# Performance work log

Hardware: AMD Instinct MI355X
Metric: run time of the kernel (lower is better)

Reference implementation:

```python
import jax, jax.numpy as jnp
import numpy as np

B, T, I, H, TGT = 256, 4096, 8, 32, 8


def setup_inputs() -> dict:
    key = jax.random.key(0)
    ks = jax.random.split(key, 6)
    return {
        "inputs": jax.random.normal(ks[0], (B, T, I), jnp.float32),
        "encode_weights": jax.random.normal(ks[1], (H, I), jnp.float32) * 0.3,   # xavier-ish
        "w_ih": jax.random.normal(ks[2], (3 * H, H), jnp.float32) * 0.1,        # GRU weight_ih_l0
        "w_hh": jax.random.normal(ks[3], (3 * H, H), jnp.float32) * 0.1,        # GRU weight_hh_l0
        "b_ih": jax.random.normal(ks[4], (3 * H,), jnp.float32) * 0.1,
        "b_hh": jax.random.normal(ks[5], (3 * H,), jnp.float32) * 0.1,
    }


def _gru(gx_t, w_hh, b_hh, h0):
    # gx_t: time-major input-gate pre-activations [T, B, 3H]; PyTorch GRU math:
    # r = sig(gx_r + gh_r); z = sig(gx_z + gh_z); n = tanh(gx_n + r*gh_n); h = (1-z)*n + z*h
    Hd = h0.shape[-1]
    def step(h, gx):
        gh = h @ w_hh.T + b_hh                      # [B, 3H]
        r = jax.nn.sigmoid(gx[..., :Hd] + gh[..., :Hd])
        z = jax.nn.sigmoid(gx[..., Hd:2 * Hd] + gh[..., Hd:2 * Hd])
        n = jnp.tanh(gx[..., 2 * Hd:] + r * gh[..., 2 * Hd:])
        h_new = (1.0 - z) * n + z * h
        return h_new, h_new
    _, hs = jax.lax.scan(step, h0, gx_t)            # hs: [T, B, H]
    return hs


def reference(inputs, encode_weights, w_ih, w_hh, b_ih, b_hh):
    # encode = F.linear(inputs, encode_weights)
    encode = jnp.einsum('bti,hi->bth', inputs, encode_weights)      # [B, T, H]
    gx = jnp.einsum('bth,gh->btg', encode, w_ih) + b_ih             # [B, T, 3H]
    gx_t = jnp.swapaxes(gx, 0, 1)                                   # [T, B, 3H]
    h0 = jnp.zeros((inputs.shape[0], encode_weights.shape[0]), inputs.dtype)
    latents = jnp.swapaxes(_gru(gx_t, w_hh, b_hh, h0), 0, 1)        # [B, T, H]
    # tied decoder: F.linear(latents, encode_weights[:, :target_size].T)
    outputs = jnp.einsum('bth,ho->bto', latents, encode_weights[:, :TGT])
    return outputs, latents
```

## Files before the change

kernel.cpp:

```cpp
#include <hip/hip_runtime.h>
#include <hip/hip_bf16.h>
#include <cstdint>
#include <cstddef>

#define Bsz  256
#define Tn   4096
#define In   8
#define Hn   32
#define TGTn 8

typedef float v2f __attribute__((ext_vector_type(2)));

__device__ __forceinline__ v2f pk_fma(v2f a, v2f b, v2f c) {
    return __builtin_elementwise_fma(a, b, c);
}
__device__ __forceinline__ v2f pk_mul(v2f a, v2f b) { return a * b; }

template<int N>
__device__ __forceinline__ float dpp_ror(float x) {
    int xi = __float_as_int(x);
    int r = __builtin_amdgcn_update_dpp(xi, xi, 0x120 + N, 0xF, 0xF, false);
    return __int_as_float(r);
}

__device__ __forceinline__ float half_sum(float x) {
    auto r = __builtin_amdgcn_permlane32_swap(__float_as_int(x), __float_as_int(x),
                                              false, false);
    return __int_as_float((int)r[0]) + __int_as_float((int)r[1]);
}

__device__ __forceinline__ void row16_pair(float x, float& a_out, float& b_out) {
    auto r = __builtin_amdgcn_permlane16_swap(__float_as_int(x), __float_as_int(x),
                                              false, false);
    a_out = __int_as_float((int)r[0]);
    b_out = __int_as_float((int)r[1]);
}

__device__ __forceinline__ void gather16_probe(float v, v2f H[8]) {
    v2f G0; G0.x = v;                G0.y = dpp_ror<1>(v);
    v2f G1; G1.x = dpp_ror<2>(G0.x); G1.y = dpp_ror<2>(G0.y);
    v2f G2; G2.x = dpp_ror<4>(G0.x); G2.y = dpp_ror<4>(G0.y);
    v2f G3; G3.x = dpp_ror<4>(G1.x); G3.y = dpp_ror<4>(G1.y);
    v2f G4; G4.x = dpp_ror<8>(G0.x); G4.y = dpp_ror<8>(G0.y);
    v2f G5; G5.x = dpp_ror<8>(G1.x); G5.y = dpp_ror<8>(G1.y);
    v2f G6; G6.x = dpp_ror<8>(G2.x); G6.y = dpp_ror<8>(G2.y);
    v2f G7; G7.x = dpp_ror<8>(G3.x); G7.y = dpp_ror<8>(G3.y);
    H[0]=G0; H[1]=G1; H[2]=G2; H[3]=G3; H[4]=G4; H[5]=G5; H[6]=G6; H[7]=G7;
}

__device__ __forceinline__ float rcpf(float x) { return __builtin_amdgcn_rcpf(x); }
__device__ __forceinline__ float sigm(float x) { return rcpf(1.f + __expf(-x)); }
__device__ __forceinline__ float tanhfast(float x) {
    float e = __expf(2.f * x);
    return 1.f - 2.f * rcpf(e + 1.f);
}

__global__ void fuse_wih_kernel(const float* __restrict__ w_ih,
                                const float* __restrict__ E,
                                float* __restrict__ Wf) {
    int tid = threadIdx.x;
    int g = tid >> 3, i = tid & 7;
    float acc = 0.f;
#pragma unroll
    for (int k = 0; k < Hn; ++k)
        acc = fmaf(w_ih[g * Hn + k], E[k * In + i], acc);
    Wf[g * In + i] = acc;
}

#define GRU_STEP(XNEXT, XREFILL, DO_REFILL)                                          \
  {                                                                                  \
    v2f ar0 = pk_fma(H0, whr0, pk_fma(H2, whr2, pk_fma(H4, whr4, pk_mul(H6, whr6))));\
    v2f ar1 = pk_fma(H1, whr1, pk_fma(H3, whr3, pk_fma(H5, whr5, pk_mul(H7, whr7))));\
    v2f az0 = pk_fma(H0, whz0, pk_fma(H2, whz2, pk_fma(H4, whz4, pk_mul(H6, whz6))));\
    v2f az1 = pk_fma(H1, whz1, pk_fma(H3, whz3, pk_fma(H5, whz5, pk_mul(H7, whz7))));\
    v2f an0 = pk_fma(H0, whn0, pk_fma(H2, whn2, pk_fma(H4, whn4, pk_mul(H6, whn6))));\
    v2f an1 = pk_fma(H1, whn1, pk_fma(H3, whn3, pk_fma(H5, whn5, pk_mul(H7, whn7))));\
    v2f art = ar0 + ar1;                                                             \
    v2f azt = az0 + az1;                                                             \
    v2f ant = an0 + an1;                                                             \
    float pr  = art.x + art.y + axr;                                                 \
    float pz  = azt.x + azt.y + axz;                                                 \
    float phn = ant.x + ant.y + bhnh;                                                \
    float cr  = half_sum(pr);                                                        \
    float cz  = half_sum(pz);                                                        \
    float chn = half_sum(phn);                                                       \
    float r = sigm(cr);                                                              \
    float z = sigm(cz);                                                              \
    float n = tanhfast(cxn + r * chn);                                               \
    hj = __builtin_fmaf(z, hj - n, n);                                               \
    float va, vb;                                                                    \
    row16_pair(hj, va, vb);                                                          \
    float gv = pick_a ? va : vb;                        \
    H0 = v2f{gv, dpp_ror<1>(gv)};                                                    \
    H1 = v2f{dpp_ror<2>(H0.x), dpp_ror<2>(H0.y)};                                    \
    H2 = v2f{dpp_ror<4>(H0.x), dpp_ror<4>(H0.y)};                                    \
    H3 = v2f{dpp_ror<4>(H1.x), dpp_ror<4>(H1.y)};                                    \
    H4 = v2f{dpp_ror<8>(H0.x), dpp_ror<8>(H0.y)};                                    \
    H5 = v2f{dpp_ror<8>(H1.x), dpp_ror<8>(H1.y)};                                    \
    H6 = v2f{dpp_ror<8>(H2.x), dpp_ror<8>(H2.y)};                                    \
    H7 = v2f{dpp_ror<8>(H3.x), dpp_ror<8>(H3.y)};                                    \
    *latp = hj;                                                                      \
    latp += Hn;                                                                      \
    {                                                                                \
      v2f nx0 = v2f{XNEXT.x, XNEXT.y}, nx1 = v2f{XNEXT.z, XNEXT.w};                  \
      v2f ta = pk_fma(nx0, wxr0, pk_mul(nx1, wxr1));                                 \
      axr = ta.x + ta.y + brh;                                                       \
      v2f tb = pk_fma(nx0, wxz0, pk_mul(nx1, wxz1));                                 \
      axz = tb.x + tb.y + bzh;                                                       \
      v2f tc = pk_fma(nx0, wxn0, pk_mul(nx1, wxn1));                                 \
      cxn = half_sum(tc.x + tc.y + bxnh);                                            \
    }                                                                                \
    if (DO_REFILL) { XREFILL = *(const float4*)refp; refp += In; }                   \
  }

#define KEEP(v) asm volatile("" : "+v"(v))
__attribute__((amdgpu_flat_work_group_size(64, 64), amdgpu_waves_per_eu(1, 1)))
__global__ void gru_kernel(const float* __restrict__ x,
                           const float* __restrict__ Wf,
                           const float* __restrict__ w_hh,
                           const float* __restrict__ b_ih,
                           const float* __restrict__ b_hh,
                           float* __restrict__ latents) {
    const int lane = threadIdx.x & 63;
    const int grp  = lane >> 5;
    const int j    = lane & 31;
    const int r16  = lane & 15;
    const int b    = blockIdx.x;

    int sidx[16];
    {
        v2f P[8];
        gather16_probe((float)r16, P);
#pragma unroll
        for (int q = 0; q < 8; ++q) {
            sidx[2*q]   = (int)P[q].x;
            sidx[2*q+1] = (int)P[q].y;
        }
    }
    bool pick_a;
    {
        float va, vb;
        row16_pair((float)j, va, vb);
        pick_a = ((int)va == grp * 16 + r16);
    }

    v2f whr0, whr1, whr2, whr3, whr4, whr5, whr6, whr7;
    v2f whz0, whz1, whz2, whz3, whz4, whz5, whz6, whz7;
    v2f whn0, whn1, whn2, whn3, whn4, whn5, whn6, whn7;
#define LOADW(Q)                                                                  \
    {                                                                             \
        const int c0 = grp * 16 + sidx[2*Q], c1 = grp * 16 + sidx[2*Q+1];         \
        whr##Q = v2f{w_hh[(0*Hn + j)*Hn + c0], w_hh[(0*Hn + j)*Hn + c1]};         \
        whz##Q = v2f{w_hh[(1*Hn + j)*Hn + c0], w_hh[(1*Hn + j)*Hn + c1]};         \
        whn##Q = v2f{w_hh[(2*Hn + j)*Hn + c0], w_hh[(2*Hn + j)*Hn + c1]};         \
        KEEP(whr##Q); KEEP(whz##Q); KEEP(whn##Q);                                 \
    }
    LOADW(0) LOADW(1) LOADW(2) LOADW(3) LOADW(4) LOADW(5) LOADW(6) LOADW(7)
#undef LOADW

    v2f wxr0 = v2f{Wf[(0*Hn+j)*In + grp*4 + 0], Wf[(0*Hn+j)*In + grp*4 + 1]};
    v2f wxr1 = v2f{Wf[(0*Hn+j)*In + grp*4 + 2], Wf[(0*Hn+j)*In + grp*4 + 3]};
    v2f wxz0 = v2f{Wf[(1*Hn+j)*In + grp*4 + 0], Wf[(1*Hn+j)*In + grp*4 + 1]};
    v2f wxz1 = v2f{Wf[(1*Hn+j)*In + grp*4 + 2], Wf[(1*Hn+j)*In + grp*4 + 3]};
    v2f wxn0 = v2f{Wf[(2*Hn+j)*In + grp*4 + 0], Wf[(2*Hn+j)*In + grp*4 + 1]};
    v2f wxn1 = v2f{Wf[(2*Hn+j)*In + grp*4 + 2], Wf[(2*Hn+j)*In + grp*4 + 3]};
    KEEP(wxr0); KEEP(wxr1); KEEP(wxz0); KEEP(wxz1); KEEP(wxn0); KEEP(wxn1);

    float brh  = 0.5f * (b_ih[j]        + b_hh[j]);
    float bzh  = 0.5f * (b_ih[Hn + j]   + b_hh[Hn + j]);
    float bxnh = 0.5f * b_ih[2*Hn + j];
    float bhnh = 0.5f * b_hh[2*Hn + j];
    KEEP(brh); KEEP(bzh); KEEP(bxnh); KEEP(bhnh);

    const float* xb = x + (size_t)b * Tn * In;
    float* latp     = latents + (size_t)b * Tn * Hn + j;
    const float* refp = xb + (size_t)8 * In + grp * 4;

    float hj = 0.f;
    v2f H0{0.f,0.f}, H1{0.f,0.f}, H2{0.f,0.f}, H3{0.f,0.f},
        H4{0.f,0.f}, H5{0.f,0.f}, H6{0.f,0.f}, H7{0.f,0.f};

    float4 x0 = *(const float4*)&xb[0*In + grp*4];
    float4 x1 = *(const float4*)&xb[1*In + grp*4];
    float4 x2 = *(const float4*)&xb[2*In + grp*4];
    float4 x3 = *(const float4*)&xb[3*In + grp*4];
    float4 x4 = *(const float4*)&xb[4*In + grp*4];
    float4 x5 = *(const float4*)&xb[5*In + grp*4];
    float4 x6 = *(const float4*)&xb[6*In + grp*4];
    float4 x7 = *(const float4*)&xb[7*In + grp*4];

    float axr, axz, cxn;
    {
        v2f nx0 = v2f{x0.x, x0.y}, nx1 = v2f{x0.z, x0.w};
        v2f ta = pk_fma(nx0, wxr0, pk_mul(nx1, wxr1));
        axr = ta.x + ta.y + brh;
        v2f tb = pk_fma(nx0, wxz0, pk_mul(nx1, wxz1));
        axz = tb.x + tb.y + bzh;
        v2f tc = pk_fma(nx0, wxn0, pk_mul(nx1, wxn1));
        cxn = half_sum(tc.x + tc.y + bxnh);
    }

#pragma unroll 1
    for (int s0 = 0; s0 < Tn - 8; s0 += 8) {
        GRU_STEP(x1, x0, true)
        GRU_STEP(x2, x1, true)
        GRU_STEP(x3, x2, true)
        GRU_STEP(x4, x3, true)
        GRU_STEP(x5, x4, true)
        GRU_STEP(x6, x5, true)
        GRU_STEP(x7, x6, true)
        GRU_STEP(x0, x7, true)
    }
    GRU_STEP(x1, x0, false)
    GRU_STEP(x2, x1, false)
    GRU_STEP(x3, x2, false)
    GRU_STEP(x4, x3, false)
    GRU_STEP(x5, x4, false)
    GRU_STEP(x6, x5, false)
    GRU_STEP(x7, x6, false)
    GRU_STEP(x0, x7, false)
}
#undef KEEP

__global__ void decode_kernel(const float* __restrict__ lat,
                              const float* __restrict__ E,
                              float* __restrict__ out) {
    __shared__ float ldsE[Hn * TGTn];
    int tid = threadIdx.x;
    if (tid < Hn * TGTn) ldsE[tid] = E[tid];
    __syncthreads();
    size_t idx = (size_t)blockIdx.x * 256 + tid;
    int o      = (int)(idx & (TGTn - 1));
    size_t row = idx >> 3;
    const float* lrow = lat + row * Hn;
    float acc = 0.f;
#pragma unroll
    for (int h = 0; h < Hn; ++h)
        acc = fmaf(lrow[h], ldsE[h * TGTn + o], acc);
    out[idx] = acc;
}

extern "C" void kernel_launch(void* const* d_in, const int* in_sizes, int n_in,
                              void* d_out, int out_size, void* d_ws, size_t ws_size,
                              hipStream_t stream) {
    const float* x    = (const float*)d_in[0];
    const float* E    = (const float*)d_in[1];
    const float* w_ih = (const float*)d_in[2];
    const float* w_hh = (const float*)d_in[3];
    const float* b_ih = (const float*)d_in[4];
    const float* b_hh = (const float*)d_in[5];

    float* out = (float*)d_out;
    float* lat = out + (size_t)Bsz * Tn * TGTn;
    float* Wf  = (float*)d_ws;

    fuse_wih_kernel<<<1, 768, 0, stream>>>(w_ih, E, Wf);
    gru_kernel<<<Bsz, 64, 0, stream>>>(x, Wf, w_hh, b_ih, b_hh, lat);
    decode_kernel<<<(Bsz * Tn * TGTn) / 256, 256, 0, stream>>>(lat, E, out);
}
```

Baseline: 992.5 us.

## Prescale GRU weights for exp2 activations and compute full input preact per lane

Folds the -log2(e) and 2*log2(e) factors into w_hh, the fused input weights and the biases, so sigmoid and tanh become a raw exp2 plus reciprocal with no extra multiply. Each lane now computes the full 8-wide input pre-activation itself rather than splitting it across the two half-waves and combining with a permlane swap. That removes one cross-lane swap from the serial recurrence, at the cost of more FMAs and twice the x loads per lane. The x prefetch ring shrinks from 8 to 4 timesteps, which lowers register use but shortens the load lead time.

```diff
diff --git a/kernel.cpp b/kernel.cpp
--- a/kernel.cpp
+++ b/kernel.cpp
@@ -9,12 +9,21 @@
 #define Hn   32
 #define TGTn 8
 
+#define ALPHA (-1.44269504088896341f)
+#define BETA  ( 2.88539008177792682f)
+
 typedef float v2f __attribute__((ext_vector_type(2)));
 
 __device__ __forceinline__ v2f pk_fma(v2f a, v2f b, v2f c) {
     return __builtin_elementwise_fma(a, b, c);
 }
-__device__ __forceinline__ v2f pk_mul(v2f a, v2f b) { return a * b; }
+
+#if __has_builtin(__builtin_amdgcn_exp2f)
+__device__ __forceinline__ float exp2f_fast(float x) { return __builtin_amdgcn_exp2f(x); }
+#else
+__device__ __forceinline__ float exp2f_fast(float x) { return __expf(x * 0.69314718056f); }
+#endif
+__device__ __forceinline__ float rcpf(float x) { return __builtin_amdgcn_rcpf(x); }
 
 template<int N>
 __device__ __forceinline__ float dpp_ror(float x) {
@@ -48,13 +57,6 @@
     H[0]=G0; H[1]=G1; H[2]=G2; H[3]=G3; H[4]=G4; H[5]=G5; H[6]=G6; H[7]=G7;
 }
 
-__device__ __forceinline__ float rcpf(float x) { return __builtin_amdgcn_rcpf(x); }
-__device__ __forceinline__ float sigm(float x) { return rcpf(1.f + __expf(-x)); }
-__device__ __forceinline__ float tanhfast(float x) {
-    float e = __expf(2.f * x);
-    return 1.f - 2.f * rcpf(e + 1.f);
-}
-
 __global__ void fuse_wih_kernel(const float* __restrict__ w_ih,
                                 const float* __restrict__ E,
                                 float* __restrict__ Wf) {
@@ -64,29 +66,40 @@
 #pragma unroll
     for (int k = 0; k < Hn; ++k)
         acc = fmaf(w_ih[g * Hn + k], E[k * In + i], acc);
-    Wf[g * In + i] = acc;
-}
-
-#define GRU_STEP(XNEXT, XREFILL, DO_REFILL)                                          \
+    Wf[g * In + i] = acc * (g < 2 * Hn ? ALPHA : BETA);
+}
+
+#define PREACT(XA, XB)                                                               \
   {                                                                                  \
-    v2f ar0 = pk_fma(H0, whr0, pk_fma(H2, whr2, pk_fma(H4, whr4, pk_mul(H6, whr6))));\
-    v2f ar1 = pk_fma(H1, whr1, pk_fma(H3, whr3, pk_fma(H5, whr5, pk_mul(H7, whr7))));\
-    v2f az0 = pk_fma(H0, whz0, pk_fma(H2, whz2, pk_fma(H4, whz4, pk_mul(H6, whz6))));\
-    v2f az1 = pk_fma(H1, whz1, pk_fma(H3, whz3, pk_fma(H5, whz5, pk_mul(H7, whz7))));\
-    v2f an0 = pk_fma(H0, whn0, pk_fma(H2, whn2, pk_fma(H4, whn4, pk_mul(H6, whn6))));\
-    v2f an1 = pk_fma(H1, whn1, pk_fma(H3, whn3, pk_fma(H5, whn5, pk_mul(H7, whn7))));\
+    v2f p0 = v2f{XA.x, XA.y}, p1 = v2f{XA.z, XA.w};                                  \
+    v2f p2 = v2f{XB.x, XB.y}, p3 = v2f{XB.z, XB.w};                                  \
+    v2f dr = pk_fma(p0, wxr0, pk_fma(p1, wxr1, pk_fma(p2, wxr2, pk_fma(p3, wxr3, biasr)))); \
+    axr = dr.x + dr.y;                                                               \
+    v2f dz = pk_fma(p0, wxz0, pk_fma(p1, wxz1, pk_fma(p2, wxz2, pk_fma(p3, wxz3, biasz)))); \
+    axz = dz.x + dz.y;                                                               \
+    v2f dn = pk_fma(p0, wxn0, pk_fma(p1, wxn1, pk_fma(p2, wxn2, pk_fma(p3, wxn3, biasn)))); \
+    cxn = dn.x + dn.y;                                                               \
+  }
+
+#define GRU_STEP(XNA, XNB, XRA, XRB, DO_REFILL)                                      \
+  {                                                                                  \
+    v2f ar0 = pk_fma(H0, whr0, pk_fma(H2, whr2, pk_fma(H4, whr4, H6 * whr6)));       \
+    v2f ar1 = pk_fma(H1, whr1, pk_fma(H3, whr3, pk_fma(H5, whr5, H7 * whr7)));       \
+    v2f az0 = pk_fma(H0, whz0, pk_fma(H2, whz2, pk_fma(H4, whz4, H6 * whz6)));       \
+    v2f az1 = pk_fma(H1, whz1, pk_fma(H3, whz3, pk_fma(H5, whz5, H7 * whz7)));       \
+    v2f an0 = pk_fma(H0, whn0, pk_fma(H2, whn2, pk_fma(H4, whn4, H6 * whn6)));       \
+    v2f an1 = pk_fma(H1, whn1, pk_fma(H3, whn3, pk_fma(H5, whn5, H7 * whn7)));       \
     v2f art = ar0 + ar1;                                                             \
     v2f azt = az0 + az1;                                                             \
     v2f ant = an0 + an1;                                                             \
-    float pr  = art.x + art.y + axr;                                                 \
-    float pz  = azt.x + azt.y + axz;                                                 \
-    float phn = ant.x + ant.y + bhnh;                                                \
-    float cr  = half_sum(pr);                                                        \
-    float cz  = half_sum(pz);                                                        \
-    float chn = half_sum(phn);                                                       \
-    float r = sigm(cr);                                                              \
-    float z = sigm(cz);                                                              \
-    float n = tanhfast(cxn + r * chn);                                               \
+    float cr  = half_sum(art.x + art.y) + axr;                                       \
+    float cz  = half_sum(azt.x + azt.y) + axz;                                       \
+    float chn = half_sum(ant.x + ant.y) + bhnB;                                      \
+    float r = rcpf(1.f + exp2f_fast(cr));                                            \
+    float z = rcpf(1.f + exp2f_fast(cz));                                            \
+    float e = exp2f_fast(__builtin_fmaf(r, chn, cxn));                               \
+    float u = rcpf(e + 1.f);                                                         \
+    float n = __builtin_fmaf(-2.f, u, 1.f);                                          \
     hj = __builtin_fmaf(z, hj - n, n);                                               \
     float va, vb;                                                                    \
     row16_pair(hj, va, vb);                                                          \
@@ -99,18 +112,14 @@
     H5 = v2f{dpp_ror<8>(H1.x), dpp_ror<8>(H1.y)};                                    \
     H6 = v2f{dpp_ror<8>(H2.x), dpp_ror<8>(H2.y)};                                    \
     H7 = v2f{dpp_ror<8>(H3.x), dpp_ror<8>(H3.y)};                                    \
-    *latp = hj;                                                                      \
-    latp += Hn;                                                                      \
-    {                                                                                \
-      v2f nx0 = v2f{XNEXT.x, XNEXT.y}, nx1 = v2f{XNEXT.z, XNEXT.w};                  \
-      v2f ta = pk_fma(nx0, wxr0, pk_mul(nx1, wxr1));                                 \
-      axr = ta.x + ta.y + brh;                                                       \
-      v2f tb = pk_fma(nx0, wxz0, pk_mul(nx1, wxz1));                                 \
-      axz = tb.x + tb.y + bzh;                                                       \
-      v2f tc = pk_fma(nx0, wxn0, pk_mul(nx1, wxn1));                                 \
-      cxn = half_sum(tc.x + tc.y + bxnh);                                            \
+    latb[j] = hj;                                                                    \
+    latb += Hn;                                                 \
+    PREACT(XNA, XNB)                                                                 \
+    if (DO_REFILL) {                                                                 \
+        XRA = *(const float4*)(refp);                                                \
+        XRB = *(const float4*)(refp + 4);                                            \
+        refp += In;                                             \
     }                                                                                \
-    if (DO_REFILL) { XREFILL = *(const float4*)refp; refp += In; }                   \
   }
 
 #define KEEP(v) asm volatile("" : "+v"(v))
@@ -147,78 +156,60 @@
     v2f whr0, whr1, whr2, whr3, whr4, whr5, whr6, whr7;
     v2f whz0, whz1, whz2, whz3, whz4, whz5, whz6, whz7;
     v2f whn0, whn1, whn2, whn3, whn4, whn5, whn6, whn7;
-#define LOADW(Q)                                                                  \
-    {                                                                             \
-        const int c0 = grp * 16 + sidx[2*Q], c1 = grp * 16 + sidx[2*Q+1];         \
-        whr##Q = v2f{w_hh[(0*Hn + j)*Hn + c0], w_hh[(0*Hn + j)*Hn + c1]};         \
-        whz##Q = v2f{w_hh[(1*Hn + j)*Hn + c0], w_hh[(1*Hn + j)*Hn + c1]};         \
-        whn##Q = v2f{w_hh[(2*Hn + j)*Hn + c0], w_hh[(2*Hn + j)*Hn + c1]};         \
-        KEEP(whr##Q); KEEP(whz##Q); KEEP(whn##Q);                                 \
+#define LOADW(Q)                                                                     \
+    {                                                                                \
+        const int c0 = grp * 16 + sidx[2*Q], c1 = grp * 16 + sidx[2*Q+1];            \
+        whr##Q = v2f{ALPHA * w_hh[(0*Hn + j)*Hn + c0], ALPHA * w_hh[(0*Hn + j)*Hn + c1]}; \
+        whz##Q = v2f{ALPHA * w_hh[(1*Hn + j)*Hn + c0], ALPHA * w_hh[(1*Hn + j)*Hn + c1]}; \
+        whn##Q = v2f{BETA  * w_hh[(2*Hn + j)*Hn + c0], BETA  * w_hh[(2*Hn + j)*Hn + c1]}; \
+        KEEP(whr##Q); KEEP(whz##Q); KEEP(whn##Q);                                    \
     }
     LOADW(0) LOADW(1) LOADW(2) LOADW(3) LOADW(4) LOADW(5) LOADW(6) LOADW(7)
 #undef LOADW
 
-    v2f wxr0 = v2f{Wf[(0*Hn+j)*In + grp*4 + 0], Wf[(0*Hn+j)*In + grp*4 + 1]};
-    v2f wxr1 = v2f{Wf[(0*Hn+j)*In + grp*4 + 2], Wf[(0*Hn+j)*In + grp*4 + 3]};
-    v2f wxz0 = v2f{Wf[(1*Hn+j)*In + grp*4 + 0], Wf[(1*Hn+j)*In + grp*4 + 1]};
-    v2f wxz1 = v2f{Wf[(1*Hn+j)*In + grp*4 + 2], Wf[(1*Hn+j)*In + grp*4 + 3]};
-    v2f wxn0 = v2f{Wf[(2*Hn+j)*In + grp*4 + 0], Wf[(2*Hn+j)*In + grp*4 + 1]};
-    v2f wxn1 = v2f{Wf[(2*Hn+j)*In + grp*4 + 2], Wf[(2*Hn+j)*In + grp*4 + 3]};
-    KEEP(wxr0); KEEP(wxr1); KEEP(wxz0); KEEP(wxz1); KEEP(wxn0); KEEP(wxn1);
-
-    float brh  = 0.5f * (b_ih[j]        + b_hh[j]);
-    float bzh  = 0.5f * (b_ih[Hn + j]   + b_hh[Hn + j]);
-    float bxnh = 0.5f * b_ih[2*Hn + j];
-    float bhnh = 0.5f * b_hh[2*Hn + j];
-    KEEP(brh); KEEP(bzh); KEEP(bxnh); KEEP(bhnh);
+    v2f wxr0 = *(const v2f*)&Wf[(0*Hn+j)*In + 0], wxr1 = *(const v2f*)&Wf[(0*Hn+j)*In + 2];
+    v2f wxr2 = *(const v2f*)&Wf[(0*Hn+j)*In + 4], wxr3 = *(const v2f*)&Wf[(0*Hn+j)*In + 6];
+    v2f wxz0 = *(const v2f*)&Wf[(1*Hn+j)*In + 0], wxz1 = *(const v2f*)&Wf[(1*Hn+j)*In + 2];
+    v2f wxz2 = *(const v2f*)&Wf[(1*Hn+j)*In + 4], wxz3 = *(const v2f*)&Wf[(1*Hn+j)*In + 6];
+    v2f wxn0 = *(const v2f*)&Wf[(2*Hn+j)*In + 0], wxn1 = *(const v2f*)&Wf[(2*Hn+j)*In + 2];
+    v2f wxn2 = *(const v2f*)&Wf[(2*Hn+j)*In + 4], wxn3 = *(const v2f*)&Wf[(2*Hn+j)*In + 6];
+    KEEP(wxr0); KEEP(wxr1); KEEP(wxr2); KEEP(wxr3);
+    KEEP(wxz0); KEEP(wxz1); KEEP(wxz2); KEEP(wxz3);
+    KEEP(wxn0); KEEP(wxn1); KEEP(wxn2); KEEP(wxn3);
+
+    v2f biasr = v2f{ALPHA * (b_ih[j]      + b_hh[j]),      0.f};
+    v2f biasz = v2f{ALPHA * (b_ih[Hn + j] + b_hh[Hn + j]), 0.f};
+    v2f biasn = v2f{BETA  *  b_ih[2*Hn + j],               0.f};
+    float bhnB = BETA * b_hh[2*Hn + j];
+    KEEP(biasr); KEEP(biasz); KEEP(biasn); KEEP(bhnB);
 
     const float* xb = x + (size_t)b * Tn * In;
-    float* latp     = latents + (size_t)b * Tn * Hn + j;
-    const float* refp = xb + (size_t)8 * In + grp * 4;
+    float* latb     = latents + (size_t)b * Tn * Hn;
+    const float* refp = xb + 4 * In;
 
     float hj = 0.f;
     v2f H0{0.f,0.f}, H1{0.f,0.f}, H2{0.f,0.f}, H3{0.f,0.f},
         H4{0.f,0.f}, H5{0.f,0.f}, H6{0.f,0.f}, H7{0.f,0.f};
 
-    float4 x0 = *(const float4*)&xb[0*In + grp*4];
-    float4 x1 = *(const float4*)&xb[1*In + grp*4];
-    float4 x2 = *(const float4*)&xb[2*In + grp*4];
-    float4 x3 = *(const float4*)&xb[3*In + grp*4];
-    float4 x4 = *(const float4*)&xb[4*In + grp*4];
-    float4 x5 = *(const float4*)&xb[5*In + grp*4];
-    float4 x6 = *(const float4*)&xb[6*In + grp*4];
-    float4 x7 = *(const float4*)&xb[7*In + grp*4];
+    float4 a0 = *(const float4*)&xb[0*In],     b0 = *(const float4*)&xb[0*In + 4];
+    float4 a1 = *(const float4*)&xb[1*In],     b1 = *(const float4*)&xb[1*In + 4];
+    float4 a2 = *(const float4*)&xb[2*In],     b2 = *(const float4*)&xb[2*In + 4];
+    float4 a3 = *(const float4*)&xb[3*In],     b3 = *(const float4*)&xb[3*In + 4];
 
     float axr, axz, cxn;
-    {
-        v2f nx0 = v2f{x0.x, x0.y}, nx1 = v2f{x0.z, x0.w};
-        v2f ta = pk_fma(nx0, wxr0, pk_mul(nx1, wxr1));
-        axr = ta.x + ta.y + brh;
-        v2f tb = pk_fma(nx0, wxz0, pk_mul(nx1, wxz1));
-        axz = tb.x + tb.y + bzh;
-        v2f tc = pk_fma(nx0, wxn0, pk_mul(nx1, wxn1));
-        cxn = half_sum(tc.x + tc.y + bxnh);
-    }
+    PREACT(a0, b0)
 
 #pragma unroll 1
-    for (int s0 = 0; s0 < Tn - 8; s0 += 8) {
-        GRU_STEP(x1, x0, true)
-        GRU_STEP(x2, x1, true)
-        GRU_STEP(x3, x2, true)
-        GRU_STEP(x4, x3, true)
-        GRU_STEP(x5, x4, true)
-        GRU_STEP(x6, x5, true)
-        GRU_STEP(x7, x6, true)
-        GRU_STEP(x0, x7, true)
-    }
-    GRU_STEP(x1, x0, false)
-    GRU_STEP(x2, x1, false)
-    GRU_STEP(x3, x2, false)
-    GRU_STEP(x4, x3, false)
-    GRU_STEP(x5, x4, false)
-    GRU_STEP(x6, x5, false)
-    GRU_STEP(x7, x6, false)
-    GRU_STEP(x0, x7, false)
+    for (int s0 = 0; s0 < Tn - 4; s0 += 4) {
+        GRU_STEP(a1, b1, a0, b0, true)
+        GRU_STEP(a2, b2, a1, b1, true)
+        GRU_STEP(a3, b3, a2, b2, true)
+        GRU_STEP(a0, b0, a3, b3, true)
+    }
+    GRU_STEP(a1, b1, a0, b0, false)
+    GRU_STEP(a2, b2, a1, b1, false)
+    GRU_STEP(a3, b3, a2, b2, false)
+    GRU_STEP(a0, b0, a3, b3, false)
 }
 #undef KEEP
 
```

After: 1.170 ms. +17.8%, slower.

## Precompute input-gate projections in chunked kernel and stream them into GRU recurrence

Applied to the files above, without the earlier changes.

Moves the input-to-gate projection out of the serial GRU loop into a separate parallel gx kernel, run over time chunks sized to fit the workspace. The recurrent kernel then reads the precomputed r/z/n pre-activations from memory and carries the hidden state between chunk launches through a global buffer. The dot products are also reshaped into single long FMA chains instead of two split halves. The aim is to shorten the per-step critical path, at the cost of extra global traffic for gx, several extra kernel launches, and a longer dependent FMA chain per gate.

```diff
diff --git a/kernel.cpp b/kernel.cpp
--- a/kernel.cpp
+++ b/kernel.cpp
@@ -67,27 +67,37 @@
     Wf[g * In + i] = acc;
 }
 
-#define GRU_STEP(XNEXT, XREFILL, DO_REFILL)                                          \
+__global__ void gx_kernel(const float* __restrict__ x,
+                          const float* __restrict__ Wf,
+                          const float* __restrict__ b_ih,
+                          const float* __restrict__ b_hh,
+                          float* __restrict__ gx,
+                          int t0, int Tc) {
+    int local = blockIdx.x * 256 + threadIdx.x;
+    int b     = blockIdx.y;
+    int j     = local & 31;
+    int trel  = local >> 5;
+    const float* xr = x + ((size_t)b * Tn + t0 + trel) * In;
+    float x0 = xr[0], x1 = xr[1], x2 = xr[2], x3 = xr[3],
+          x4 = xr[4], x5 = xr[5], x6 = xr[6], x7 = xr[7];
+    const float* wr = &Wf[(0 * Hn + j) * In];
+    const float* wz = &Wf[(1 * Hn + j) * In];
+    const float* wn = &Wf[(2 * Hn + j) * In];
+    float ar = b_ih[j] + b_hh[j];
+    float az = b_ih[Hn + j] + b_hh[Hn + j];
+    float an = b_ih[2 * Hn + j];
+    ar = fmaf(wr[0],x0,ar); ar = fmaf(wr[1],x1,ar); ar = fmaf(wr[2],x2,ar); ar = fmaf(wr[3],x3,ar);
+    ar = fmaf(wr[4],x4,ar); ar = fmaf(wr[5],x5,ar); ar = fmaf(wr[6],x6,ar); ar = fmaf(wr[7],x7,ar);
+    az = fmaf(wz[0],x0,az); az = fmaf(wz[1],x1,az); az = fmaf(wz[2],x2,az); az = fmaf(wz[3],x3,az);
+    az = fmaf(wz[4],x4,az); az = fmaf(wz[5],x5,az); az = fmaf(wz[6],x6,az); az = fmaf(wz[7],x7,az);
+    an = fmaf(wn[0],x0,an); an = fmaf(wn[1],x1,an); an = fmaf(wn[2],x2,an); an = fmaf(wn[3],x3,an);
+    an = fmaf(wn[4],x4,an); an = fmaf(wn[5],x5,an); an = fmaf(wn[6],x6,an); an = fmaf(wn[7],x7,an);
+    float* o = gx + (((size_t)b * Tc + trel) * Hn + j) * 3;
+    o[0] = ar; o[1] = az; o[2] = an;
+}
+
+#define BCAST()                                                                      \
   {                                                                                  \
-    v2f ar0 = pk_fma(H0, whr0, pk_fma(H2, whr2, pk_fma(H4, whr4, pk_mul(H6, whr6))));\
-    v2f ar1 = pk_fma(H1, whr1, pk_fma(H3, whr3, pk_fma(H5, whr5, pk_mul(H7, whr7))));\
-    v2f az0 = pk_fma(H0, whz0, pk_fma(H2, whz2, pk_fma(H4, whz4, pk_mul(H6, whz6))));\
-    v2f az1 = pk_fma(H1, whz1, pk_fma(H3, whz3, pk_fma(H5, whz5, pk_mul(H7, whz7))));\
-    v2f an0 = pk_fma(H0, whn0, pk_fma(H2, whn2, pk_fma(H4, whn4, pk_mul(H6, whn6))));\
-    v2f an1 = pk_fma(H1, whn1, pk_fma(H3, whn3, pk_fma(H5, whn5, pk_mul(H7, whn7))));\
-    v2f art = ar0 + ar1;                                                             \
-    v2f azt = az0 + az1;                                                             \
-    v2f ant = an0 + an1;                                                             \
-    float pr  = art.x + art.y + axr;                                                 \
-    float pz  = azt.x + azt.y + axz;                                                 \
-    float phn = ant.x + ant.y + bhnh;                                                \
-    float cr  = half_sum(pr);                                                        \
-    float cz  = half_sum(pz);                                                        \
-    float chn = half_sum(phn);                                                       \
-    float r = sigm(cr);                                                              \
-    float z = sigm(cz);                                                              \
-    float n = tanhfast(cxn + r * chn);                                               \
-    hj = __builtin_fmaf(z, hj - n, n);                                               \
     float va, vb;                                                                    \
     row16_pair(hj, va, vb);                                                          \
     float gv = pick_a ? va : vb;                        \
@@ -99,28 +109,38 @@
     H5 = v2f{dpp_ror<8>(H1.x), dpp_ror<8>(H1.y)};                                    \
     H6 = v2f{dpp_ror<8>(H2.x), dpp_ror<8>(H2.y)};                                    \
     H7 = v2f{dpp_ror<8>(H3.x), dpp_ror<8>(H3.y)};                                    \
+  }
+
+#define GRU_STEP(GA, GB, GC)                                                         \
+  {                                                                                  \
+    v2f ar = pk_fma(H0, whr0, pk_fma(H1, whr1, pk_fma(H2, whr2, pk_fma(H3, whr3,     \
+             pk_fma(H4, whr4, pk_fma(H5, whr5, pk_fma(H6, whr6, pk_mul(H7, whr7)))))))); \
+    v2f az = pk_fma(H0, whz0, pk_fma(H1, whz1, pk_fma(H2, whz2, pk_fma(H3, whz3,     \
+             pk_fma(H4, whz4, pk_fma(H5, whz5, pk_fma(H6, whz6, pk_mul(H7, whz7)))))))); \
+    v2f an = pk_fma(H0, whn0, pk_fma(H1, whn1, pk_fma(H2, whn2, pk_fma(H3, whn3,     \
+             pk_fma(H4, whn4, pk_fma(H5, whn5, pk_fma(H6, whn6, pk_mul(H7, whn7)))))))); \
+    float cr  = half_sum(ar.x + ar.y) + GA;                                          \
+    float cz  = half_sum(az.x + az.y) + GB;                                          \
+    float chn = half_sum(an.x + an.y) + bhn;                                         \
+    float r = sigm(cr);                                                              \
+    float z = sigm(cz);                                                              \
+    float n = tanhfast(__builtin_fmaf(r, chn, GC));                                  \
+    hj = __builtin_fmaf(z, hj - n, n);                                               \
+    BCAST()                                                                          \
     *latp = hj;                                                                      \
     latp += Hn;                                                                      \
-    {                                                                                \
-      v2f nx0 = v2f{XNEXT.x, XNEXT.y}, nx1 = v2f{XNEXT.z, XNEXT.w};                  \
-      v2f ta = pk_fma(nx0, wxr0, pk_mul(nx1, wxr1));                                 \
-      axr = ta.x + ta.y + brh;                                                       \
-      v2f tb = pk_fma(nx0, wxz0, pk_mul(nx1, wxz1));                                 \
-      axz = tb.x + tb.y + bzh;                                                       \
-      v2f tc = pk_fma(nx0, wxn0, pk_mul(nx1, wxn1));                                 \
-      cxn = half_sum(tc.x + tc.y + bxnh);                                            \
-    }                                                                                \
-    if (DO_REFILL) { XREFILL = *(const float4*)refp; refp += In; }                   \
+    GA = refp[0]; GB = refp[1]; GC = refp[2];                                        \
+    refp += 3 * Hn;                                                                  \
   }
 
 #define KEEP(v) asm volatile("" : "+v"(v))
 __attribute__((amdgpu_flat_work_group_size(64, 64), amdgpu_waves_per_eu(1, 1)))
-__global__ void gru_kernel(const float* __restrict__ x,
-                           const float* __restrict__ Wf,
+__global__ void gru_kernel(const float* __restrict__ gx,
                            const float* __restrict__ w_hh,
-                           const float* __restrict__ b_ih,
                            const float* __restrict__ b_hh,
-                           float* __restrict__ latents) {
+                           float* __restrict__ hbuf,
+                           float* __restrict__ latents,
+                           int t0, int Tc, int first) {
     const int lane = threadIdx.x & 63;
     const int grp  = lane >> 5;
     const int j    = lane & 31;
@@ -158,67 +178,34 @@
     LOADW(0) LOADW(1) LOADW(2) LOADW(3) LOADW(4) LOADW(5) LOADW(6) LOADW(7)
 #undef LOADW
 
-    v2f wxr0 = v2f{Wf[(0*Hn+j)*In + grp*4 + 0], Wf[(0*Hn+j)*In + grp*4 + 1]};
-    v2f wxr1 = v2f{Wf[(0*Hn+j)*In + grp*4 + 2], Wf[(0*Hn+j)*In + grp*4 + 3]};
-    v2f wxz0 = v2f{Wf[(1*Hn+j)*In + grp*4 + 0], Wf[(1*Hn+j)*In + grp*4 + 1]};
-    v2f wxz1 = v2f{Wf[(1*Hn+j)*In + grp*4 + 2], Wf[(1*Hn+j)*In + grp*4 + 3]};
-    v2f wxn0 = v2f{Wf[(2*Hn+j)*In + grp*4 + 0], Wf[(2*Hn+j)*In + grp*4 + 1]};
-    v2f wxn1 = v2f{Wf[(2*Hn+j)*In + grp*4 + 2], Wf[(2*Hn+j)*In + grp*4 + 3]};
-    KEEP(wxr0); KEEP(wxr1); KEEP(wxz0); KEEP(wxz1); KEEP(wxn0); KEEP(wxn1);
-
-    float brh  = 0.5f * (b_ih[j]        + b_hh[j]);
-    float bzh  = 0.5f * (b_ih[Hn + j]   + b_hh[Hn + j]);
-    float bxnh = 0.5f * b_ih[2*Hn + j];
-    float bhnh = 0.5f * b_hh[2*Hn + j];
-    KEEP(brh); KEEP(bzh); KEEP(bxnh); KEEP(bhnh);
-
-    const float* xb = x + (size_t)b * Tn * In;
-    float* latp     = latents + (size_t)b * Tn * Hn + j;
-    const float* refp = xb + (size_t)8 * In + grp * 4;
-
-    float hj = 0.f;
-    v2f H0{0.f,0.f}, H1{0.f,0.f}, H2{0.f,0.f}, H3{0.f,0.f},
-        H4{0.f,0.f}, H5{0.f,0.f}, H6{0.f,0.f}, H7{0.f,0.f};
-
-    float4 x0 = *(const float4*)&xb[0*In + grp*4];
-    float4 x1 = *(const float4*)&xb[1*In + grp*4];
-    float4 x2 = *(const float4*)&xb[2*In + grp*4];
-    float4 x3 = *(const float4*)&xb[3*In + grp*4];
-    float4 x4 = *(const float4*)&xb[4*In + grp*4];
-    float4 x5 = *(const float4*)&xb[5*In + grp*4];
-    float4 x6 = *(const float4*)&xb[6*In + grp*4];
-    float4 x7 = *(const float4*)&xb[7*In + grp*4];
-
-    float axr, axz, cxn;
-    {
-        v2f nx0 = v2f{x0.x, x0.y}, nx1 = v2f{x0.z, x0.w};
-        v2f ta = pk_fma(nx0, wxr0, pk_mul(nx1, wxr1));
-        axr = ta.x + ta.y + brh;
-        v2f tb = pk_fma(nx0, wxz0, pk_mul(nx1, wxz1));
-        axz = tb.x + tb.y + bzh;
-        v2f tc = pk_fma(nx0, wxn0, pk_mul(nx1, wxn1));
-        cxn = half_sum(tc.x + tc.y + bxnh);
-    }
+    float bhn = b_hh[2 * Hn + j];
+    KEEP(bhn);
+
+    float* latp = latents + (size_t)b * Tn * Hn + (size_t)t0 * Hn + j;
+    const float* refp = gx + ((size_t)b * Tc) * (3 * Hn) + j * 3;
+
+    float hj = first ? 0.f : hbuf[b * Hn + j];
+    v2f H0, H1, H2, H3, H4, H5, H6, H7;
+    BCAST()
+
+    float g0a = refp[0], g0b = refp[1], g0c = refp[2]; refp += 3 * Hn;
+    float g1a = refp[0], g1b = refp[1], g1c = refp[2]; refp += 3 * Hn;
+    float g2a = refp[0], g2b = refp[1], g2c = refp[2]; refp += 3 * Hn;
+    float g3a = refp[0], g3b = refp[1], g3c = refp[2]; refp += 3 * Hn;
 
 #pragma unroll 1
-    for (int s0 = 0; s0 < Tn - 8; s0 += 8) {
-        GRU_STEP(x1, x0, true)
-        GRU_STEP(x2, x1, true)
-        GRU_STEP(x3, x2, true)
-        GRU_STEP(x4, x3, true)
-        GRU_STEP(x5, x4, true)
-        GRU_STEP(x6, x5, true)
-        GRU_STEP(x7, x6, true)
-        GRU_STEP(x0, x7, true)
-    }
-    GRU_STEP(x1, x0, false)
-    GRU_STEP(x2, x1, false)
-    GRU_STEP(x3, x2, false)
-    GRU_STEP(x4, x3, false)
-    GRU_STEP(x5, x4, false)
-    GRU_STEP(x6, x5, false)
-    GRU_STEP(x7, x6, false)
-    GRU_STEP(x0, x7, false)
+    for (int it = 0; it < Tc / 8; ++it) {
+        GRU_STEP(g0a, g0b, g0c)
+        GRU_STEP(g1a, g1b, g1c)
+        GRU_STEP(g2a, g2b, g2c)
+        GRU_STEP(g3a, g3b, g3c)
+        GRU_STEP(g0a, g0b, g0c)
+        GRU_STEP(g1a, g1b, g1c)
+        GRU_STEP(g2a, g2b, g2c)
+        GRU_STEP(g3a, g3b, g3c)
+    }
+
+    if (grp == 0) hbuf[b * Hn + j] = hj;
 }
 #undef KEEP
 
@@ -250,11 +237,23 @@
     const float* b_ih = (const float*)d_in[4];
     const float* b_hh = (const float*)d_in[5];
 
-    float* out = (float*)d_out;
-    float* lat = out + (size_t)Bsz * Tn * TGTn;
-    float* Wf  = (float*)d_ws;
+    float* out  = (float*)d_out;
+    float* lat  = out + (size_t)Bsz * Tn * TGTn;
+    float* Wf   = (float*)d_ws;
+    float* hbuf = Wf + 1024;
+    float* gx   = hbuf + Bsz * Hn;
+
+    size_t avail = (ws_size / 4 > (size_t)(1024 + Bsz * Hn))
+                 ? ws_size / 4 - (1024 + Bsz * Hn) : 0;
+    int Tc = 1024;
+    while (Tc > 8 && (size_t)Bsz * Tc * 3 * Hn + 4 * 3 * Hn > avail) Tc >>= 1;
 
     fuse_wih_kernel<<<1, 768, 0, stream>>>(w_ih, E, Wf);
-    gru_kernel<<<Bsz, 64, 0, stream>>>(x, Wf, w_hh, b_ih, b_hh, lat);
+    for (int t0 = 0; t0 < Tn; t0 += Tc) {
+        gx_kernel<<<dim3(Tc * Hn / 256, Bsz), 256, 0, stream>>>(
+            x, Wf, b_ih, b_hh, gx, t0, Tc);
+        gru_kernel<<<Bsz, 64, 0, stream>>>(
+            gx, w_hh, b_hh, hbuf, lat, t0, Tc, t0 == 0 ? 1 : 0);
+    }
     decode_kernel<<<(Bsz * Tn * TGTn) / 256, 256, 0, stream>>>(lat, E, out);
 }
```

Result: slower. 1.099 ms (+10.7%).
